# Kernel tuning notes

Hardware: AMD Instinct MI355X
Metric: run time of the kernel (lower is better)

Reference implementation:

```python
import jax, jax.numpy as jnp
import numpy as np

B = 4096


def setup_inputs() -> dict:
    key = jax.random.key(0)
    u = jax.random.uniform(key, (B, 5), dtype=jnp.float32)
    centers = u[:, :2] * 64.0          # box centers in [0, 64)
    wh = u[:, 2:4] * 8.0 + 1.0         # widths/heights in [1, 9)
    ang = u[:, 4:5] * 3.14159265       # rotation angle in [0, pi)
    boxes = jnp.concatenate([centers, wh, ang], axis=-1)  # (B,5)
    return {"boxes": boxes}


def _rect_to_corners(boxes):
    # boxes: (B,5) = (x, y, w, h, theta) -> corners (B,4,2)
    unit = jnp.array([[-1.0, -1.0], [1.0, -1.0], [1.0, 1.0], [-1.0, 1.0]],
                     dtype=boxes.dtype)
    ctr, wh, ang = boxes[:, :2], boxes[:, 2:4], boxes[:, 4]
    base = unit[None, :, :] * (wh * 0.5)[:, None, :]        # (B,4,2)
    c, s = jnp.cos(ang), jnp.sin(ang)
    rot = jnp.stack([jnp.stack([c, -s], -1),
                     jnp.stack([s, c], -1)], axis=1)         # (B,2,2)
    return jnp.einsum('bkd,bde->bke', base, rot) + ctr[:, None, :]


def _giou1d(min1, max1, min2, max2):
    # exact (non-fast) 1-D GIoU per axis
    inter = jnp.clip(jnp.minimum(max1, max2) - jnp.maximum(min1, min2), 0.0)
    union = (max1 - min1) + (max2 - min2) - inter
    hull = jnp.maximum(max1, max2) - jnp.minimum(min1, min2)
    return inter / union - (hull - union) / hull


def reference(boxes):
    corners = _rect_to_corners(boxes)                        # (B,4,2)
    nb = corners.shape[0]
    # two edge axes per box: c1-c0 and c3-c0
    axes = jnp.stack([corners[:, 1] - corners[:, 0],
                      corners[:, 3] - corners[:, 0]], axis=1)  # (B,2,2)
    # self projections: box b's corners onto its own axes
    sp = jnp.einsum('bkd,bad->bak', corners, axes)           # (B,2,4)
    smin, smax = sp.min(-1), sp.max(-1)                      # (B,2)
    # cross projections: corners of box i onto axes of box j
    cp = jnp.einsum('ikd,jad->ijak', corners, axes)          # (B,B,2,4)
    cmin, cmax = cp.min(-1), cp.max(-1)                      # (B,B,2)
    # projections of box j's corners onto box i's axes = transpose of cross
    cminT, cmaxT = jnp.swapaxes(cmin, 0, 1), jnp.swapaxes(cmax, 0, 1)
    # axes of box i: (box i self) vs (box j projected on i's axes)
    gA = _giou1d(smin[:, None, :], smax[:, None, :], cminT, cmaxT)  # (B,B,2)
    # axes of box j: (box i projected on j's axes) vs (box j self)
    gB = _giou1d(cmin, cmax, smin[None, :, :], smax[None, :, :])    # (B,B,2)
    g = jnp.concatenate([gA, gB], axis=-1).min(-1)           # min over 4 axes
    pairwise = jnp.clip(g, 0.0)
    idx = jnp.arange(nb)
    pairwise = pairwise.at[idx, idx].set(0.0)                # zero diagonal
    return pairwise  # reduction='none' -> (B,B)
```

## Files before the change

### kernel.cpp

```cpp
#include <hip/hip_runtime.h>
#include <math.h>

#define NBOX 4096
#define TILE 32
#define NT (NBOX / TILE)
#define NBLK (NT * (NT + 1) / 2)
#define SS 12


struct Box {
    float c0x, c0y, a0x, a0y, a1x, a1y;
    float smin0, smax0, len0, smin1, smax1, len1;
};

__device__ __forceinline__ float rcp_fast(float x) {
    return __builtin_amdgcn_rcpf(x);
}

__device__ __forceinline__ float giou_axis(float wx, float wy,
                                           float smin, float smax, float slen,
                                           const Box& Q) {
    float p0 = fmaf(wx, Q.c0x, wy * Q.c0y);
    float da = fmaf(wx, Q.a0x, wy * Q.a0y);
    float db = fmaf(wx, Q.a1x, wy * Q.a1y);
    float mn = p0 + fminf(da, 0.0f) + fminf(db, 0.0f);
    float len2 = fabsf(da) + fabsf(db);
    float mx = mn + len2;
    float r = fminf(smax, mx) - fmaxf(smin, mn);
    float L = slen + len2;
    return r * rcp_fast(L - r);
}

__device__ __forceinline__ float mgiou_pair(const Box& I, const Box& J) {
    float g0 = giou_axis(I.a0x, I.a0y, I.smin0, I.smax0, I.len0, J);
    float g1 = giou_axis(I.a1x, I.a1y, I.smin1, I.smax1, I.len1, J);
    float g2 = giou_axis(J.a0x, J.a0y, J.smin0, J.smax0, J.len0, I);
    float g3 = giou_axis(J.a1x, J.a1y, J.smin1, J.smax1, J.len1, I);
    float g = fminf(fminf(g0, g1), fminf(g2, g3));
    return fmaxf(g, 0.0f);
}

__device__ __forceinline__ Box load_box(const float* __restrict__ p) {
    Box b;
    float4 x = *(const float4*)(p);
    float4 y = *(const float4*)(p + 4);
    float4 z = *(const float4*)(p + 8);
    b.c0x = x.x; b.c0y = x.y; b.a0x = x.z; b.a0y = x.w;
    b.a1x = y.x; b.a1y = y.y; b.smin0 = y.z; b.smax0 = y.w;
    b.len0 = z.x; b.smin1 = z.y; b.smax1 = z.z; b.len1 = z.w;
    return b;
}

__global__ __launch_bounds__(256)
void pairwise_kernel(const float* __restrict__ boxes, float* __restrict__ out) {
    int k = blockIdx.x;
    int bi = (int)((float)(2 * NT + 1 - sqrtf((float)((2 * NT + 1) * (2 * NT + 1) - 8 * k))) * 0.5f);
    if (bi > 0 && k < bi * NT - bi * (bi - 1) / 2) bi--;
    if (k >= (bi + 1) * NT - (bi + 1) * bi / 2) bi++;
    int bj = bi + (k - (bi * NT - bi * (bi - 1) / 2));

    __shared__ float sm[2 * TILE][SS];
    __shared__ float tileT[TILE][TILE + 1];

    int tid = threadIdx.x;
    if (tid < 2 * TILE) {
        int box = (tid < TILE) ? (bi * TILE + tid) : (bj * TILE + (tid - TILE));
        float cx = boxes[box * 5 + 0];
        float cy = boxes[box * 5 + 1];
        float hw = boxes[box * 5 + 2] * 0.5f;
        float hh = boxes[box * 5 + 3] * 0.5f;
        float ang = boxes[box * 5 + 4];
        float s, c;
        __sincosf(ang, &s, &c);
        float e0x = hw * c, e0y = -hw * s;
        float e1x = hh * s, e1y =  hh * c;
        float c0x = cx - e0x - e1x, c0y = cy - e0y - e1y;
        float a0x = 2.0f * e0x, a0y = 2.0f * e0y;
        float a1x = 2.0f * e1x, a1y = 2.0f * e1y;
        float l0 = fmaf(a0x, a0x, a0y * a0y);
        float l1 = fmaf(a1x, a1x, a1y * a1y);
        float smin0 = fmaf(a0x, c0x, a0y * c0y);
        float smin1 = fmaf(a1x, c0x, a1y * c0y);
        float* d = &sm[tid][0];
        d[0] = c0x; d[1] = c0y; d[2] = a0x; d[3] = a0y;
        d[4] = a1x; d[5] = a1y; d[6] = smin0; d[7] = smin0 + l0;
        d[8] = l0;  d[9] = smin1; d[10] = smin1 + l1; d[11] = l1;
    }
    __syncthreads();

    int tx = tid & 15;
    int ty = tid >> 4;
    Box I0 = load_box(&sm[ty][0]);
    Box I1 = load_box(&sm[ty + 16][0]);
    Box J0 = load_box(&sm[TILE + tx][0]);
    Box J1 = load_box(&sm[TILE + tx + 16][0]);

    int ig0 = bi * TILE + ty, ig1 = ig0 + 16;
    int jg0 = bj * TILE + tx, jg1 = jg0 + 16;

    float v00 = (ig0 == jg0) ? 0.0f : mgiou_pair(I0, J0);
    float v01 = (ig0 == jg1) ? 0.0f : mgiou_pair(I0, J1);
    float v10 = (ig1 == jg0) ? 0.0f : mgiou_pair(I1, J0);
    float v11 = (ig1 == jg1) ? 0.0f : mgiou_pair(I1, J1);

    out[(size_t)ig0 * NBOX + jg0] = v00;
    out[(size_t)ig0 * NBOX + jg1] = v01;
    out[(size_t)ig1 * NBOX + jg0] = v10;
    out[(size_t)ig1 * NBOX + jg1] = v11;

    tileT[ty][tx]           = v00;
    tileT[ty][tx + 16]      = v01;
    tileT[ty + 16][tx]      = v10;
    tileT[ty + 16][tx + 16] = v11;
    __syncthreads();

    int ibase = bi * TILE;
    int jbase = bj * TILE;
    #pragma unroll
    for (int dr = 0; dr < 2; ++dr) {
        int jl = ty + dr * 16;
        #pragma unroll
        for (int dc = 0; dc < 2; ++dc) {
            int il = tx + dc * 16;
            out[(size_t)(jbase + jl) * NBOX + (ibase + il)] = tileT[il][jl];
        }
    }
}

extern "C" void kernel_launch(void* const* d_in, const int* in_sizes, int n_in,
                              void* d_out, int out_size, void* d_ws, size_t ws_size,
                              hipStream_t stream) {
    const float* boxes = (const float*)d_in[0];
    float* out = (float*)d_out;
    pairwise_kernel<<<dim3(NBLK), dim3(256), 0, stream>>>(boxes, out);
}
```

Measured before the change: 88.47 us.

## Reformulate per-axis GIoU via center distance and half-extents, vectorize stores

Each 1-D projection overlap is rewritten using center-offset and extent sums, so the four axis tests share four axis dot products instead of computing corner projections per axis. The per-box record shrinks from 12 to 10 floats and J records are padded in shared memory to reduce bank conflicts. Global writes become float2 stores with each thread covering adjacent columns. The reformulated maths may differ slightly in floating-point rounding from the original projection approach.

```diff
diff --git a/kernel.cpp b/kernel.cpp
--- a/kernel.cpp
+++ b/kernel.cpp
@@ -6,48 +6,57 @@
 #define NT (NBOX / TILE)
 #define NBLK (NT * (NT + 1) / 2)
 #define SS 12
+#define JBASE (TILE * SS)
 
 
 struct Box {
-    float c0x, c0y, a0x, a0y, a1x, a1y;
-    float smin0, smax0, len0, smin1, smax1, len1;
+    float cx, cy, a0x, a0y, a1x, a1y, sc0, sc1, l0, l1;
 };
 
 __device__ __forceinline__ float rcp_fast(float x) {
     return __builtin_amdgcn_rcpf(x);
 }
 
-__device__ __forceinline__ float giou_axis(float wx, float wy,
-                                           float smin, float smax, float slen,
-                                           const Box& Q) {
-    float p0 = fmaf(wx, Q.c0x, wy * Q.c0y);
-    float da = fmaf(wx, Q.a0x, wy * Q.a0y);
-    float db = fmaf(wx, Q.a1x, wy * Q.a1y);
-    float mn = p0 + fminf(da, 0.0f) + fminf(db, 0.0f);
-    float len2 = fabsf(da) + fabsf(db);
-    float mx = mn + len2;
-    float r = fminf(smax, mx) - fmaxf(smin, mn);
-    float L = slen + len2;
-    return r * rcp_fast(L - r);
+__device__ __forceinline__ float giou_axis1(float H1, float H2, float D) {
+    float S = H1 + H2;
+    float u = fmaf(0.5f, S, -fabsf(D));
+    float r = fminf(fminf(H1, H2), u);
+    return r * rcp_fast(S - r);
 }
 
 __device__ __forceinline__ float mgiou_pair(const Box& I, const Box& J) {
-    float g0 = giou_axis(I.a0x, I.a0y, I.smin0, I.smax0, I.len0, J);
-    float g1 = giou_axis(I.a1x, I.a1y, I.smin1, I.smax1, I.len1, J);
-    float g2 = giou_axis(J.a0x, J.a0y, J.smin0, J.smax0, J.len0, I);
-    float g3 = giou_axis(J.a1x, J.a1y, J.smin1, J.smax1, J.len1, I);
+    float d00 = fmaf(I.a0x, J.a0x, I.a0y * J.a0y);
+    float d01 = fmaf(I.a0x, J.a1x, I.a0y * J.a1y);
+    float d10 = fmaf(I.a1x, J.a0x, I.a1y * J.a0y);
+    float d11 = fmaf(I.a1x, J.a1x, I.a1y * J.a1y);
+    float DI0 = fmaf(I.a0x, J.cx, fmaf(I.a0y, J.cy, -I.sc0));
+    float DI1 = fmaf(I.a1x, J.cx, fmaf(I.a1y, J.cy, -I.sc1));
+    float DJ0 = fmaf(J.a0x, I.cx, fmaf(J.a0y, I.cy, -J.sc0));
+    float DJ1 = fmaf(J.a1x, I.cx, fmaf(J.a1y, I.cy, -J.sc1));
+    float HI0 = fabsf(d00) + fabsf(d01);
+    float HI1 = fabsf(d10) + fabsf(d11);
+    float HJ0 = fabsf(d00) + fabsf(d10);
+    float HJ1 = fabsf(d01) + fabsf(d11);
+    float g0 = giou_axis1(I.l0, HI0, DI0);
+    float g1 = giou_axis1(I.l1, HI1, DI1);
+    float g2 = giou_axis1(J.l0, HJ0, DJ0);
+    float g3 = giou_axis1(J.l1, HJ1, DJ1);
     float g = fminf(fminf(g0, g1), fminf(g2, g3));
     return fmaxf(g, 0.0f);
 }
 
-__device__ __forceinline__ Box load_box(const float* __restrict__ p) {
+__device__ __forceinline__ int j_offset(int j) {
+    return JBASE + j * SS + (j >> 3) * 4;
+}
+
+__device__ __forceinline__ Box load_box(const float* p) {
     Box b;
     float4 x = *(const float4*)(p);
     float4 y = *(const float4*)(p + 4);
-    float4 z = *(const float4*)(p + 8);
-    b.c0x = x.x; b.c0y = x.y; b.a0x = x.z; b.a0y = x.w;
-    b.a1x = y.x; b.a1y = y.y; b.smin0 = y.z; b.smax0 = y.w;
-    b.len0 = z.x; b.smin1 = z.y; b.smax1 = z.z; b.len1 = z.w;
+    float2 z = *(const float2*)(p + 8);
+    b.cx = x.x;  b.cy = x.y;  b.a0x = x.z; b.a0y = x.w;
+    b.a1x = y.x; b.a1y = y.y; b.sc0 = y.z; b.sc1 = y.w;
+    b.l0 = z.x;  b.l1 = z.y;
     return b;
 }
 
@@ -59,71 +68,62 @@
     if (k >= (bi + 1) * NT - (bi + 1) * bi / 2) bi++;
     int bj = bi + (k - (bi * NT - bi * (bi - 1) / 2));
 
-    __shared__ float sm[2 * TILE][SS];
+    __shared__ float sm[JBASE + TILE * SS + 16];
     __shared__ float tileT[TILE][TILE + 1];
 
     int tid = threadIdx.x;
     if (tid < 2 * TILE) {
-        int box = (tid < TILE) ? (bi * TILE + tid) : (bj * TILE + (tid - TILE));
+        int loc = (tid < TILE) ? tid : (tid - TILE);
+        int box = (tid < TILE) ? (bi * TILE + loc) : (bj * TILE + loc);
         float cx = boxes[box * 5 + 0];
         float cy = boxes[box * 5 + 1];
-        float hw = boxes[box * 5 + 2] * 0.5f;
-        float hh = boxes[box * 5 + 3] * 0.5f;
+        float w  = boxes[box * 5 + 2];
+        float h  = boxes[box * 5 + 3];
         float ang = boxes[box * 5 + 4];
         float s, c;
         __sincosf(ang, &s, &c);
-        float e0x = hw * c, e0y = -hw * s;
-        float e1x = hh * s, e1y =  hh * c;
-        float c0x = cx - e0x - e1x, c0y = cy - e0y - e1y;
-        float a0x = 2.0f * e0x, a0y = 2.0f * e0y;
-        float a1x = 2.0f * e1x, a1y = 2.0f * e1y;
-        float l0 = fmaf(a0x, a0x, a0y * a0y);
-        float l1 = fmaf(a1x, a1x, a1y * a1y);
-        float smin0 = fmaf(a0x, c0x, a0y * c0y);
-        float smin1 = fmaf(a1x, c0x, a1y * c0y);
-        float* d = &sm[tid][0];
-        d[0] = c0x; d[1] = c0y; d[2] = a0x; d[3] = a0y;
-        d[4] = a1x; d[5] = a1y; d[6] = smin0; d[7] = smin0 + l0;
-        d[8] = l0;  d[9] = smin1; d[10] = smin1 + l1; d[11] = l1;
+        float a0x = w * c, a0y = -w * s;
+        float a1x = h * s, a1y =  h * c;
+        float sc0 = fmaf(a0x, cx, a0y * cy);
+        float sc1 = fmaf(a1x, cx, a1y * cy);
+        float* d = &sm[(tid < TILE) ? (loc * SS) : j_offset(loc)];
+        ((float4*)d)[0] = make_float4(cx, cy, a0x, a0y);
+        ((float4*)d)[1] = make_float4(a1x, a1y, sc0, sc1);
+        ((float2*)d)[4] = make_float2(w * w, h * h);
     }
     __syncthreads();
 
     int tx = tid & 15;
     int ty = tid >> 4;
-    Box I0 = load_box(&sm[ty][0]);
-    Box I1 = load_box(&sm[ty + 16][0]);
-    Box J0 = load_box(&sm[TILE + tx][0]);
-    Box J1 = load_box(&sm[TILE + tx + 16][0]);
+    Box I0 = load_box(&sm[ty * SS]);
+    Box I1 = load_box(&sm[(ty + 16) * SS]);
+    const float* jp = &sm[j_offset(2 * tx)];
+    Box J0 = load_box(jp);
+    Box J1 = load_box(jp + SS);
 
-    int ig0 = bi * TILE + ty, ig1 = ig0 + 16;
-    int jg0 = bj * TILE + tx, jg1 = jg0 + 16;
+    int ibase = bi * TILE, jbase = bj * TILE;
+    int ig0 = ibase + ty, ig1 = ig0 + 16;
+    int jg0 = jbase + 2 * tx, jg1 = jg0 + 1;
 
     float v00 = (ig0 == jg0) ? 0.0f : mgiou_pair(I0, J0);
     float v01 = (ig0 == jg1) ? 0.0f : mgiou_pair(I0, J1);
     float v10 = (ig1 == jg0) ? 0.0f : mgiou_pair(I1, J0);
     float v11 = (ig1 == jg1) ? 0.0f : mgiou_pair(I1, J1);
 
-    out[(size_t)ig0 * NBOX + jg0] = v00;
-    out[(size_t)ig0 * NBOX + jg1] = v01;
-    out[(size_t)ig1 * NBOX + jg0] = v10;
-    out[(size_t)ig1 * NBOX + jg1] = v11;
+    *(float2*)&out[(size_t)ig0 * NBOX + jg0] = make_float2(v00, v01);
+    *(float2*)&out[(size_t)ig1 * NBOX + jg0] = make_float2(v10, v11);
 
-    tileT[ty][tx]           = v00;
-    tileT[ty][tx + 16]      = v01;
-    tileT[ty + 16][tx]      = v10;
-    tileT[ty + 16][tx + 16] = v11;
+    tileT[ty][2 * tx]          = v00;
+    tileT[ty][2 * tx + 1]      = v01;
+    tileT[ty + 16][2 * tx]     = v10;
+    tileT[ty + 16][2 * tx + 1] = v11;
     __syncthreads();
 
-    int ibase = bi * TILE;
-    int jbase = bj * TILE;
     #pragma unroll
     for (int dr = 0; dr < 2; ++dr) {
         int jl = ty + dr * 16;
-        #pragma unroll
-        for (int dc = 0; dc < 2; ++dc) {
-            int il = tx + dc * 16;
-            out[(size_t)(jbase + jl) * NBOX + (ibase + il)] = tileT[il][jl];
-        }
+        float2 o = make_float2(tileT[2 * tx][jl], tileT[2 * tx + 1][jl]);
+        *(float2*)&out[(size_t)(jbase + jl) * NBOX + ibase + 2 * tx] = o;
     }
 }
 
```

After: 82.11 us. 1.08x faster.
